# Kernel tuning notes

Measured on AMD Instinct MI355X. Metric: run time of the kernel, lower is better.

The kernel has to match this reference:

```python
import jax, jax.numpy as jnp
import numpy as np
from jax import lax

BS, H, W, C, V = 64, 32, 32, 684, 128
N, NP, Q, E, HID = 256, 512, 256, 256, 256  # n, n_prime, decoder_conv_filters, embedding_dim, hidden_size


def setup_inputs() -> dict:
    key = jax.random.key(0)
    ks = jax.random.split(key, 20)
    s = 0.02
    d = {}
    d["x"] = jax.random.randint(ks[0], (BS, 1), 0, V)
    d["hidden"] = jax.random.normal(ks[1], (1, BS, HID), jnp.float32)
    d["feature"] = jax.random.normal(ks[2], (BS, C, H, W), jnp.float32)
    d["alpha"] = jax.random.uniform(ks[3], (BS, 1, H * W), jnp.float32)
    d["emb"] = jax.random.normal(ks[4], (V, E), jnp.float32) * s
    d["gru1_wih"] = jax.random.normal(ks[5], (3 * HID, E), jnp.float32) * s
    d["gru1_whh"] = jax.random.normal(ks[6], (3 * HID, HID), jnp.float32) * s
    d["gru1_bih"] = jnp.zeros((3 * HID,), jnp.float32)
    d["gru1_bhh"] = jnp.zeros((3 * HID,), jnp.float32)
    d["gru2_wih"] = jax.random.normal(ks[7], (3 * HID, C), jnp.float32) * s
    d["gru2_whh"] = jax.random.normal(ks[8], (3 * HID, HID), jnp.float32) * s
    d["gru2_bih"] = jnp.zeros((3 * HID,), jnp.float32)
    d["gru2_bhh"] = jnp.zeros((3 * HID,), jnp.float32)
    d["convQ_w"] = jax.random.normal(ks[9], (Q, 1, 11, 11), jnp.float32) * s
    d["convQ_b"] = jnp.zeros((Q,), jnp.float32)
    d["Wa_w"] = jax.random.normal(ks[10], (NP, N), jnp.float32) * s
    d["Wa_b"] = jnp.zeros((NP,), jnp.float32)
    d["Ua_w"] = jax.random.normal(ks[11], (NP, C), jnp.float32) * s
    d["Ua_b"] = jnp.zeros((NP,), jnp.float32)
    d["Uf_w"] = jax.random.normal(ks[12], (NP, Q), jnp.float32) * s
    d["Uf_b"] = jnp.zeros((NP,), jnp.float32)
    d["Va_w"] = jax.random.normal(ks[13], (1, NP), jnp.float32) * s
    d["Va_b"] = jnp.zeros((1,), jnp.float32)
    d["Ws_w"] = jax.random.normal(ks[14], (E, HID), jnp.float32) * s
    d["Ws_b"] = jnp.zeros((E,), jnp.float32)
    d["Wc_w"] = jax.random.normal(ks[15], (E, C), jnp.float32) * s
    d["Wc_b"] = jnp.zeros((E,), jnp.float32)
    d["Wo_w"] = jax.random.normal(ks[16], (V, E // 2), jnp.float32) * s
    d["Wo_b"] = jnp.zeros((V,), jnp.float32)
    return d


def gru_step(x, h, w_ih, w_hh, b_ih, b_hh):
    """PyTorch nn.GRU single-step cell."""
    gi = x @ w_ih.T + b_ih
    gh = h @ w_hh.T + b_hh
    ir, iz, in_ = jnp.split(gi, 3, axis=-1)
    hr, hz, hn = jnp.split(gh, 3, axis=-1)
    r = jax.nn.sigmoid(ir + hr)
    z = jax.nn.sigmoid(iz + hz)
    n = jnp.tanh(in_ + r * hn)
    return (1.0 - z) * n + z * h


def reference(x, hidden, feature, alpha, emb,
              gru1_wih, gru1_whh, gru1_bih, gru1_bhh,
              gru2_wih, gru2_whh, gru2_bih, gru2_bhh,
              convQ_w, convQ_b, Wa_w, Wa_b, Ua_w, Ua_b,
              Uf_w, Uf_b, Va_w, Va_b, Ws_w, Ws_b, Wc_w, Wc_b, Wo_w, Wo_b):
    bs, c, h, w = feature.shape
    embedded = emb[x[:, 0]]                                   # [bs, E]
    pred = gru_step(embedded, hidden[0], gru1_wih, gru1_whh, gru1_bih, gru1_bhh)  # [bs, HID]

    # --- coverage attention ---
    beta = alpha.sum(1).reshape(bs, 1, h, w)                  # coverage map
    Fmap = lax.conv_general_dilated(beta, convQ_w, (1, 1), [(5, 5), (5, 5)],
                                    dimension_numbers=("NCHW", "OIHW", "NCHW"))
    Fmap = Fmap + convQ_b[None, :, None, None]                # [bs, Q, h, w]
    cover = jnp.einsum("bqhw,pq->bhwp", Fmap, Uf_w) + Uf_b    # [bs, h, w, NP]
    key_t = jnp.einsum("bchw,pc->bhwp", feature, Ua_w) + Ua_b # 1x1 conv_Ua
    query = pred @ Wa_w.T + Wa_b                              # [bs, NP]
    score = jnp.tanh(key_t + cover + query[:, None, None, :]) # [bs, h, w, NP]
    e_t = (jnp.einsum("bhwp,p->bhw", score, Va_w[0]) + Va_b[0]).reshape(bs, -1)
    e_exp = jnp.exp(e_t)                                      # faithful: exp/sum + 1e-8 (no max-shift)
    alpha_t = e_exp / (e_exp.sum(1, keepdims=True) + 1e-8)    # [bs, h*w]
    context = jnp.einsum("bcl,bl->bc", feature.reshape(bs, c, -1), alpha_t)  # [bs, C]

    # --- second GRU + output head ---
    h2 = gru_step(context, pred, gru2_wih, gru2_whh, gru2_bih, gru2_bhh)  # [bs, HID]
    o = embedded + (h2 @ Ws_w.T + Ws_b) + (context @ Wc_w.T + Wc_b)       # [bs, E]
    o = o.reshape(bs, -1, 2).max(-1)                                       # maxout pool 2
    logits = o @ Wo_w.T + Wo_b                                             # [bs, V]
    return logits, h2[:, None, :], alpha_t.reshape(bs, 1, h, w)
```

## Files before the change

kernel.cpp:

```cpp
#include <hip/hip_runtime.h>
#include <hip/hip_bf16.h>
#include <math.h>

#define BSZ 64
#define HGT 32
#define WID 32
#define HWN 1024
#define CCH 684
#define KP 704
#define VOC 128
#define NPP 512
#define QCH 256
#define EMB 256
#define HID 256
#define TAPP 128

typedef __attribute__((ext_vector_type(8))) short short8v;
typedef __attribute__((ext_vector_type(4))) float f32x4;

__device__ __forceinline__ float sigmoid_(float x) {
    return 1.0f / (1.0f + __expf(-x));
}
__device__ __forceinline__ float tanh_(float x) {
    x = fminf(fmaxf(x, -30.0f), 30.0f);
    float e = __expf(2.0f * x);
    return (e - 1.0f) / (e + 1.0f);
}
__device__ __forceinline__ unsigned short f2bf(float f) {
    unsigned int u = __float_as_uint(f);
    u = (u + 0x7FFFu + ((u >> 16) & 1u)) >> 16;
    return (unsigned short)u;
}

__global__ __launch_bounds__(256) void k_prep_ua(const float* __restrict__ Ua_w,
                                                 unsigned short* __restrict__ Ua_bf) {
    int p = blockIdx.x;
    for (int c = threadIdx.x; c < KP; c += 256) {
        unsigned short v = 0;
        if (c < CCH) v = f2bf(Ua_w[p * CCH + c]);
        Ua_bf[p * KP + c] = v;
    }
}

__global__ __launch_bounds__(256) void k_fold_w2(const float* __restrict__ Uf_w,
                                                 const float* __restrict__ Uf_b,
                                                 const float* __restrict__ convQ_w,
                                                 const float* __restrict__ convQ_b,
                                                 unsigned short* __restrict__ W2_bf,
                                                 float* __restrict__ covb) {
    int tap = blockIdx.x;
    int t = threadIdx.x;
    if (tap < TAPP) {
        for (int p = t; p < NPP; p += 256) {
            unsigned short v = 0;
            if (tap < 121) {
                float s = 0.f;
                for (int q = 0; q < QCH; q++) s += Uf_w[p * QCH + q] * convQ_w[q * 121 + tap];
                v = f2bf(s);
            }
            W2_bf[p * TAPP + tap] = v;
        }
    } else {
        for (int p = t; p < NPP; p += 256) {
            float s = Uf_b[p];
            for (int q = 0; q < QCH; q++) s += convQ_b[q] * Uf_w[p * QCH + q];
            covb[p] = s;
        }
    }
}

__global__ __launch_bounds__(256) void k_embed_gru1(const int* __restrict__ x,
                                                    const float* __restrict__ hidden,
                                                    const float* __restrict__ emb,
                                                    const float* __restrict__ w_ih,
                                                    const float* __restrict__ w_hh,
                                                    const float* __restrict__ b_ih,
                                                    const float* __restrict__ b_hh,
                                                    const float* __restrict__ Wa_w,
                                                    const float* __restrict__ Wa_b,
                                                    const float* __restrict__ covb,
                                                    const float* __restrict__ Ua_b,
                                                    float* __restrict__ ws_emb,
                                                    float* __restrict__ ws_pred,
                                                    float* __restrict__ ws_q0) {
    int b = blockIdx.x, t = threadIdx.x;
    __shared__ float se[EMB], sh[HID], sp[HID];
    int xi = x[b];
    se[t] = emb[xi * EMB + t];
    sh[t] = hidden[b * HID + t];
    __syncthreads();

    const float* wr = w_ih + (size_t)t * EMB;
    const float* wz = w_ih + (size_t)(t + 256) * EMB;
    const float* wn = w_ih + (size_t)(t + 512) * EMB;
    const float* vr = w_hh + (size_t)t * HID;
    const float* vz = w_hh + (size_t)(t + 256) * HID;
    const float* vn = w_hh + (size_t)(t + 512) * HID;
    float ir = 0, iz = 0, in_ = 0, hr = 0, hz = 0, hn = 0;
    for (int k = 0; k < EMB; k += 4) {
        float4 a0 = *(const float4*)(wr + k);
        float4 a1 = *(const float4*)(wz + k);
        float4 a2 = *(const float4*)(wn + k);
        float4 h0 = *(const float4*)(vr + k);
        float4 h1 = *(const float4*)(vz + k);
        float4 h2 = *(const float4*)(vn + k);
        float e0 = se[k], e1 = se[k + 1], e2 = se[k + 2], e3 = se[k + 3];
        float g0 = sh[k], g1 = sh[k + 1], g2 = sh[k + 2], g3 = sh[k + 3];
        ir += a0.x * e0 + a0.y * e1 + a0.z * e2 + a0.w * e3;
        iz += a1.x * e0 + a1.y * e1 + a1.z * e2 + a1.w * e3;
        in_ += a2.x * e0 + a2.y * e1 + a2.z * e2 + a2.w * e3;
        hr += h0.x * g0 + h0.y * g1 + h0.z * g2 + h0.w * g3;
        hz += h1.x * g0 + h1.y * g1 + h1.z * g2 + h1.w * g3;
        hn += h2.x * g0 + h2.y * g1 + h2.z * g2 + h2.w * g3;
    }
    float r = sigmoid_(ir + b_ih[t] + hr + b_hh[t]);
    float z = sigmoid_(iz + b_ih[256 + t] + hz + b_hh[256 + t]);
    float n = tanh_(in_ + b_ih[512 + t] + r * (hn + b_hh[512 + t]));
    float pred = (1.0f - z) * n + z * sh[t];
    ws_emb[b * EMB + t] = se[t];
    ws_pred[b * HID + t] = pred;
    sp[t] = pred;
    __syncthreads();

    for (int jj = 0; jj < 2; jj++) {
        int j = t + jj * 256;
        const float* wq = Wa_w + (size_t)j * HID;
        float q = Wa_b[j] + covb[j] + Ua_b[j];
        for (int k = 0; k < HID; k += 4) {
            float4 a = *(const float4*)(wq + k);
            q += a.x * sp[k] + a.y * sp[k + 1] + a.z * sp[k + 2] + a.w * sp[k + 3];
        }
        ws_q0[b * NPP + j] = q;
    }
}

__global__ __launch_bounds__(256, 2) void k_score(const float* __restrict__ feature,
                                                  const float* __restrict__ alpha,
                                                  const unsigned short* __restrict__ Ua_bf,
                                                  const unsigned short* __restrict__ W2_bf,
                                                  const float* __restrict__ ws_q0,
                                                  const float* __restrict__ Va_w,
                                                  const float* __restrict__ Va_b,
                                                  float* __restrict__ ws_et) {
    int rb = blockIdx.x;
    int b = blockIdx.y;
    int tid = threadIdx.x;
    int wv = tid >> 6;
    int lane = tid & 63;
    int li = lane & 15;
    int k08 = (lane >> 4) * 8;
    int pbase = wv * 128;

    __shared__ unsigned short s_a[64 * 40];
    __shared__ unsigned short s_a2[64 * 136];
    __shared__ float s_et[64];

    for (int idx = tid; idx < 64 * 128; idx += 256) {
        int hwl = idx >> 7, tap = idx & 127;
        unsigned short v = 0;
        if (tap < 121) {
            int ky = tap / 11, kx = tap - ky * 11;
            int hwg = rb * 64 + hwl;
            int y = (hwg >> 5) + ky - 5;
            int xx = (hwg & 31) + kx - 5;
            if (y >= 0 && y < HGT && xx >= 0 && xx < WID)
                v = f2bf(alpha[b * HWN + y * WID + xx]);
        }
        s_a2[hwl * 136 + tap] = v;
    }
    if (tid < 64) s_et[tid] = 0.f;

    f32x4 acc[4][8];
#pragma unroll
    for (int mt = 0; mt < 4; mt++)
#pragma unroll
        for (int nt = 0; nt < 8; nt++) acc[mt][nt] = (f32x4){0.f, 0.f, 0.f, 0.f};

    const float* fbase = feature + (size_t)b * CCH * HWN + rb * 64;
    int p2 = tid & 15, g = tid >> 4;
    unsigned int* s_a_u32 = (unsigned int*)s_a;

    for (int s = 0; s < 22; s++) {
        int c0 = s * 32;
        __syncthreads();
        {
            int c1 = c0 + 2 * p2;
            float4 f0 = make_float4(0.f, 0.f, 0.f, 0.f), f1 = f0;
            if (c1 < CCH) {
                f0 = *(const float4*)(fbase + (size_t)c1 * HWN + g * 4);
                f1 = *(const float4*)(fbase + (size_t)(c1 + 1) * HWN + g * 4);
            }
            s_a_u32[(g * 4 + 0) * 20 + p2] = (unsigned int)f2bf(f0.x) | ((unsigned int)f2bf(f1.x) << 16);
            s_a_u32[(g * 4 + 1) * 20 + p2] = (unsigned int)f2bf(f0.y) | ((unsigned int)f2bf(f1.y) << 16);
            s_a_u32[(g * 4 + 2) * 20 + p2] = (unsigned int)f2bf(f0.z) | ((unsigned int)f2bf(f1.z) << 16);
            s_a_u32[(g * 4 + 3) * 20 + p2] = (unsigned int)f2bf(f0.w) | ((unsigned int)f2bf(f1.w) << 16);
        }
        __syncthreads();
        short8v af[4];
#pragma unroll
        for (int mt = 0; mt < 4; mt++)
            af[mt] = *reinterpret_cast<const short8v*>(&s_a[(mt * 16 + li) * 40 + k08]);
#pragma unroll
        for (int nt = 0; nt < 8; nt++) {
            short8v bv = *reinterpret_cast<const short8v*>(
                Ua_bf + (size_t)(pbase + nt * 16 + li) * KP + c0 + k08);
#pragma unroll
            for (int mt = 0; mt < 4; mt++)
                acc[mt][nt] = __builtin_amdgcn_mfma_f32_16x16x32_bf16(af[mt], bv, acc[mt][nt], 0, 0, 0);
        }
    }

#pragma unroll
    for (int s = 0; s < 4; s++) {
        int t0 = s * 32;
        short8v af[4];
#pragma unroll
        for (int mt = 0; mt < 4; mt++)
            af[mt] = *reinterpret_cast<const short8v*>(&s_a2[(mt * 16 + li) * 136 + t0 + k08]);
#pragma unroll
        for (int nt = 0; nt < 8; nt++) {
            short8v bv = *reinterpret_cast<const short8v*>(
                W2_bf + (size_t)(pbase + nt * 16 + li) * TAPP + t0 + k08);
#pragma unroll
            for (int mt = 0; mt < 4; mt++)
                acc[mt][nt] = __builtin_amdgcn_mfma_f32_16x16x32_bf16(af[mt], bv, acc[mt][nt], 0, 0, 0);
        }
    }

    float part[4][4];
#pragma unroll
    for (int mt = 0; mt < 4; mt++)
#pragma unroll
        for (int r = 0; r < 4; r++) part[mt][r] = 0.f;

#pragma unroll
    for (int nt = 0; nt < 8; nt++) {
        int p = pbase + nt * 16 + li;
        float q0 = ws_q0[b * NPP + p];
        float va = Va_w[p];
#pragma unroll
        for (int mt = 0; mt < 4; mt++)
#pragma unroll
            for (int r = 0; r < 4; r++)
                part[mt][r] += va * tanh_(acc[mt][nt][r] + q0);
    }
#pragma unroll
    for (int mask = 1; mask <= 8; mask <<= 1)
#pragma unroll
        for (int mt = 0; mt < 4; mt++)
#pragma unroll
            for (int r = 0; r < 4; r++)
                part[mt][r] += __shfl_xor(part[mt][r], mask, 64);

    if (li == 0) {
        int rb4 = (lane >> 4) * 4;
#pragma unroll
        for (int mt = 0; mt < 4; mt++)
#pragma unroll
            for (int r = 0; r < 4; r++)
                atomicAdd(&s_et[mt * 16 + rb4 + r], part[mt][r]);
    }
    __syncthreads();
    if (tid < 64) ws_et[b * HWN + rb * 64 + tid] = s_et[tid] + Va_b[0];
}

__global__ __launch_bounds__(256) void k_softmax(const float* __restrict__ ws_et,
                                                 float* __restrict__ alpha_out) {
    int b = blockIdx.x, t = threadIdx.x;
    __shared__ float red[4];
    float e[4];
    float s = 0.f;
#pragma unroll
    for (int i = 0; i < 4; i++) {
        e[i] = expf(ws_et[b * HWN + t + i * 256]);
        s += e[i];
    }
#pragma unroll
    for (int off = 32; off >= 1; off >>= 1) s += __shfl_xor(s, off, 64);
    int wid = t >> 6;
    if ((t & 63) == 0) red[wid] = s;
    __syncthreads();
    float tot = red[0] + red[1] + red[2] + red[3] + 1e-8f;
    float inv = 1.0f / tot;
#pragma unroll
    for (int i = 0; i < 4; i++) alpha_out[b * HWN + t + i * 256] = e[i] * inv;
}

__global__ __launch_bounds__(256) void k_context(const float* __restrict__ feature,
                                                 const float* __restrict__ alpha_out,
                                                 float* __restrict__ ws_ctx) {
    int b = blockIdx.x;
    int c = blockIdx.y * 4 + (threadIdx.x >> 6);
    int lane = threadIdx.x & 63;
    const float* f = feature + ((size_t)b * CCH + c) * HWN;
    const float* a = alpha_out + b * HWN;
    float s = 0.f;
    for (int k = lane; k < HWN; k += 64) s += f[k] * a[k];
#pragma unroll
    for (int off = 32; off >= 1; off >>= 1) s += __shfl_xor(s, off, 64);
    if (lane == 0) ws_ctx[b * CCH + c] = s;
}

__global__ __launch_bounds__(256) void k_final(const float* __restrict__ ws_ctx,
                                               const float* __restrict__ ws_pred,
                                               const float* __restrict__ ws_emb,
                                               const float* __restrict__ w_ih2,
                                               const float* __restrict__ w_hh2,
                                               const float* __restrict__ b_ih2,
                                               const float* __restrict__ b_hh2,
                                               const float* __restrict__ Ws_w,
                                               const float* __restrict__ Ws_b,
                                               const float* __restrict__ Wc_w,
                                               const float* __restrict__ Wc_b,
                                               const float* __restrict__ Wo_w,
                                               const float* __restrict__ Wo_b,
                                               float* __restrict__ out_logits,
                                               float* __restrict__ out_h2) {
    int b = blockIdx.x, t = threadIdx.x;
    __shared__ float sc[CCH], sp[HID], semb[EMB], sh2[HID], so[EMB], som[VOC];
    for (int i = t; i < CCH; i += 256) sc[i] = ws_ctx[b * CCH + i];
    sp[t] = ws_pred[b * HID + t];
    semb[t] = ws_emb[b * EMB + t];
    __syncthreads();

    const float* wr = w_ih2 + (size_t)t * CCH;
    const float* wz = w_ih2 + (size_t)(t + 256) * CCH;
    const float* wn = w_ih2 + (size_t)(t + 512) * CCH;
    float ir = 0, iz = 0, in_ = 0;
    for (int k = 0; k < CCH; k += 4) {
        float4 a0 = *(const float4*)(wr + k);
        float4 a1 = *(const float4*)(wz + k);
        float4 a2 = *(const float4*)(wn + k);
        float c0 = sc[k], c1 = sc[k + 1], c2 = sc[k + 2], c3 = sc[k + 3];
        ir += a0.x * c0 + a0.y * c1 + a0.z * c2 + a0.w * c3;
        iz += a1.x * c0 + a1.y * c1 + a1.z * c2 + a1.w * c3;
        in_ += a2.x * c0 + a2.y * c1 + a2.z * c2 + a2.w * c3;
    }
    const float* vr = w_hh2 + (size_t)t * HID;
    const float* vz = w_hh2 + (size_t)(t + 256) * HID;
    const float* vn = w_hh2 + (size_t)(t + 512) * HID;
    float hr = 0, hz = 0, hn = 0;
    for (int k = 0; k < HID; k += 4) {
        float4 h0 = *(const float4*)(vr + k);
        float4 h1 = *(const float4*)(vz + k);
        float4 h2v = *(const float4*)(vn + k);
        float g0 = sp[k], g1 = sp[k + 1], g2 = sp[k + 2], g3 = sp[k + 3];
        hr += h0.x * g0 + h0.y * g1 + h0.z * g2 + h0.w * g3;
        hz += h1.x * g0 + h1.y * g1 + h1.z * g2 + h1.w * g3;
        hn += h2v.x * g0 + h2v.y * g1 + h2v.z * g2 + h2v.w * g3;
    }
    float rg = sigmoid_(ir + b_ih2[t] + hr + b_hh2[t]);
    float zg = sigmoid_(iz + b_ih2[256 + t] + hz + b_hh2[256 + t]);
    float ng = tanh_(in_ + b_ih2[512 + t] + rg * (hn + b_hh2[512 + t]));
    float h2 = (1.0f - zg) * ng + zg * sp[t];
    out_h2[b * HID + t] = h2;
    sh2[t] = h2;
    __syncthreads();

    const float* ws_row = Ws_w + (size_t)t * HID;
    const float* wc_row = Wc_w + (size_t)t * CCH;
    float o = semb[t] + Ws_b[t] + Wc_b[t];
    for (int k = 0; k < HID; k += 4) {
        float4 a = *(const float4*)(ws_row + k);
        o += a.x * sh2[k] + a.y * sh2[k + 1] + a.z * sh2[k + 2] + a.w * sh2[k + 3];
    }
    for (int k = 0; k < CCH; k += 4) {
        float4 a = *(const float4*)(wc_row + k);
        o += a.x * sc[k] + a.y * sc[k + 1] + a.z * sc[k + 2] + a.w * sc[k + 3];
    }
    so[t] = o;
    __syncthreads();
    if (t < VOC) som[t] = fmaxf(so[2 * t], so[2 * t + 1]);
    __syncthreads();
    if (t < VOC) {
        const float* wo_row = Wo_w + (size_t)t * VOC;
        float lg = Wo_b[t];
        for (int k = 0; k < VOC; k += 4) {
            float4 a = *(const float4*)(wo_row + k);
            lg += a.x * som[k] + a.y * som[k + 1] + a.z * som[k + 2] + a.w * som[k + 3];
        }
        out_logits[b * VOC + t] = lg;
    }
}

extern "C" void kernel_launch(void* const* d_in, const int* in_sizes, int n_in,
                              void* d_out, int out_size, void* d_ws, size_t ws_size,
                              hipStream_t stream) {
    const int* x = (const int*)d_in[0];
    const float* hidden = (const float*)d_in[1];
    const float* feature = (const float*)d_in[2];
    const float* alpha = (const float*)d_in[3];
    const float* emb = (const float*)d_in[4];
    const float* gru1_wih = (const float*)d_in[5];
    const float* gru1_whh = (const float*)d_in[6];
    const float* gru1_bih = (const float*)d_in[7];
    const float* gru1_bhh = (const float*)d_in[8];
    const float* gru2_wih = (const float*)d_in[9];
    const float* gru2_whh = (const float*)d_in[10];
    const float* gru2_bih = (const float*)d_in[11];
    const float* gru2_bhh = (const float*)d_in[12];
    const float* convQ_w = (const float*)d_in[13];
    const float* convQ_b = (const float*)d_in[14];
    const float* Wa_w = (const float*)d_in[15];
    const float* Wa_b = (const float*)d_in[16];
    const float* Ua_w = (const float*)d_in[17];
    const float* Ua_b = (const float*)d_in[18];
    const float* Uf_w = (const float*)d_in[19];
    const float* Uf_b = (const float*)d_in[20];
    const float* Va_w = (const float*)d_in[21];
    const float* Va_b = (const float*)d_in[22];
    const float* Ws_w = (const float*)d_in[23];
    const float* Ws_b = (const float*)d_in[24];
    const float* Wc_w = (const float*)d_in[25];
    const float* Wc_b = (const float*)d_in[26];
    const float* Wo_w = (const float*)d_in[27];
    const float* Wo_b = (const float*)d_in[28];

    float* out = (float*)d_out;
    float* out_logits = out;
    float* out_h2 = out + BSZ * VOC;
    float* out_alpha = out + BSZ * VOC + BSZ * HID;

    float* ws = (float*)d_ws;
    float* ws_emb = ws;
    float* ws_pred = ws + 16384;
    float* ws_q0 = ws + 32768;
    float* ws_et = ws + 65536;
    float* ws_ctx = ws + 131072;
    float* ws_covb = ws + 175104;
    unsigned short* Ua_bf = (unsigned short*)(ws + 175616);
    unsigned short* W2_bf = (unsigned short*)(ws + 355840);

    k_prep_ua<<<NPP, 256, 0, stream>>>(Ua_w, Ua_bf);
    k_fold_w2<<<TAPP + 1, 256, 0, stream>>>(Uf_w, Uf_b, convQ_w, convQ_b, W2_bf, ws_covb);
    k_embed_gru1<<<BSZ, 256, 0, stream>>>(x, hidden, emb, gru1_wih, gru1_whh,
                                          gru1_bih, gru1_bhh, Wa_w, Wa_b,
                                          ws_covb, Ua_b,
                                          ws_emb, ws_pred, ws_q0);
    k_score<<<dim3(16, BSZ), 256, 0, stream>>>(feature, alpha, Ua_bf, W2_bf,
                                               ws_q0, Va_w, Va_b, ws_et);
    k_softmax<<<BSZ, 256, 0, stream>>>(ws_et, out_alpha);
    k_context<<<dim3(BSZ, 171), 256, 0, stream>>>(feature, out_alpha, ws_ctx);
    k_final<<<BSZ, 256, 0, stream>>>(ws_ctx, ws_pred, ws_emb, gru2_wih, gru2_whh,
                                     gru2_bih, gru2_bhh, Ws_w, Ws_b, Wc_w, Wc_b,
                                     Wo_w, Wo_b, out_logits, out_h2);
}
```

Baseline: 693.2 us.

## Coalesce GRU matvecs with warp-per-row, stage full feature tile in LDS

The GRU, attention-query and output-head matvecs now give each weight row to one wavefront. Lanes read contiguous elements and the partial sums are reduced with shuffles, replacing the old one-row-per-thread strided loads that do not coalesce. k_fold_w2 now runs one block per output channel and keeps the Uf row in shared memory. The covb bias is reduced in parallel instead of in a serial loop. k_score moves to 512 threads: it converts the whole 64x684 feature tile to bf16 in LDS once instead of 22 staged chunks with barriers. Each wave now covers 64 instead of 128 projection columns, at the cost of about 108KB of LDS, which limits occupancy.

```diff
diff --git a/kernel.cpp b/kernel.cpp
--- a/kernel.cpp
+++ b/kernel.cpp
@@ -14,6 +14,7 @@
 #define EMB 256
 #define HID 256
 #define TAPP 128
+#define SAPAD 712
 
 typedef __attribute__((ext_vector_type(8))) short short8v;
 typedef __attribute__((ext_vector_type(4))) float f32x4;
@@ -48,25 +49,25 @@
                                                  const float* __restrict__ convQ_b,
                                                  unsigned short* __restrict__ W2_bf,
                                                  float* __restrict__ covb) {
-    int tap = blockIdx.x;
+    int p = blockIdx.x;
     int t = threadIdx.x;
-    if (tap < TAPP) {
-        for (int p = t; p < NPP; p += 256) {
-            unsigned short v = 0;
-            if (tap < 121) {
-                float s = 0.f;
-                for (int q = 0; q < QCH; q++) s += Uf_w[p * QCH + q] * convQ_w[q * 121 + tap];
-                v = f2bf(s);
-            }
-            W2_bf[p * TAPP + tap] = v;
-        }
-    } else {
-        for (int p = t; p < NPP; p += 256) {
-            float s = Uf_b[p];
-            for (int q = 0; q < QCH; q++) s += convQ_b[q] * Uf_w[p * QCH + q];
-            covb[p] = s;
-        }
-    }
+    __shared__ float s_uf[QCH];
+    __shared__ float s_red[4];
+    s_uf[t] = Uf_w[p * QCH + t];
+    __syncthreads();
+    if (t < TAPP) {
+        float s = 0.f;
+        if (t < 121) {
+            for (int q = 0; q < QCH; q++) s += s_uf[q] * convQ_w[q * 121 + t];
+        }
+        W2_bf[p * TAPP + t] = (t < 121) ? f2bf(s) : (unsigned short)0;
+    }
+    float v = convQ_b[t] * s_uf[t];
+#pragma unroll
+    for (int m = 32; m >= 1; m >>= 1) v += __shfl_xor(v, m, 64);
+    if ((t & 63) == 0) s_red[t >> 6] = v;
+    __syncthreads();
+    if (t == 0) covb[p] = Uf_b[p] + s_red[0] + s_red[1] + s_red[2] + s_red[3];
 }
 
 __global__ __launch_bounds__(256) void k_embed_gru1(const int* __restrict__ x,
@@ -84,57 +85,50 @@
                                                     float* __restrict__ ws_pred,
                                                     float* __restrict__ ws_q0) {
     int b = blockIdx.x, t = threadIdx.x;
-    __shared__ float se[EMB], sh[HID], sp[HID];
-    int xi = x[b];
-    se[t] = emb[xi * EMB + t];
+    int wv = t >> 6, lane = t & 63;
+    __shared__ float se[EMB], sh[HID], gi[768], gh[768], sp[HID];
+    se[t] = emb[x[b] * EMB + t];
     sh[t] = hidden[b * HID + t];
     __syncthreads();
 
-    const float* wr = w_ih + (size_t)t * EMB;
-    const float* wz = w_ih + (size_t)(t + 256) * EMB;
-    const float* wn = w_ih + (size_t)(t + 512) * EMB;
-    const float* vr = w_hh + (size_t)t * HID;
-    const float* vz = w_hh + (size_t)(t + 256) * HID;
-    const float* vn = w_hh + (size_t)(t + 512) * HID;
-    float ir = 0, iz = 0, in_ = 0, hr = 0, hz = 0, hn = 0;
-    for (int k = 0; k < EMB; k += 4) {
-        float4 a0 = *(const float4*)(wr + k);
-        float4 a1 = *(const float4*)(wz + k);
-        float4 a2 = *(const float4*)(wn + k);
-        float4 h0 = *(const float4*)(vr + k);
-        float4 h1 = *(const float4*)(vz + k);
-        float4 h2 = *(const float4*)(vn + k);
-        float e0 = se[k], e1 = se[k + 1], e2 = se[k + 2], e3 = se[k + 3];
-        float g0 = sh[k], g1 = sh[k + 1], g2 = sh[k + 2], g3 = sh[k + 3];
-        ir += a0.x * e0 + a0.y * e1 + a0.z * e2 + a0.w * e3;
-        iz += a1.x * e0 + a1.y * e1 + a1.z * e2 + a1.w * e3;
-        in_ += a2.x * e0 + a2.y * e1 + a2.z * e2 + a2.w * e3;
-        hr += h0.x * g0 + h0.y * g1 + h0.z * g2 + h0.w * g3;
-        hz += h1.x * g0 + h1.y * g1 + h1.z * g2 + h1.w * g3;
-        hn += h2.x * g0 + h2.y * g1 + h2.z * g2 + h2.w * g3;
-    }
-    float r = sigmoid_(ir + b_ih[t] + hr + b_hh[t]);
-    float z = sigmoid_(iz + b_ih[256 + t] + hz + b_hh[256 + t]);
-    float n = tanh_(in_ + b_ih[512 + t] + r * (hn + b_hh[512 + t]));
+    for (int i = 0; i < 192; i++) {
+        int j = wv * 192 + i;
+        const float* wi = w_ih + (size_t)j * EMB;
+        const float* wh = w_hh + (size_t)j * HID;
+        float s1 = wi[lane] * se[lane] + wi[lane + 64] * se[lane + 64] +
+                   wi[lane + 128] * se[lane + 128] + wi[lane + 192] * se[lane + 192];
+        float s2 = wh[lane] * sh[lane] + wh[lane + 64] * sh[lane + 64] +
+                   wh[lane + 128] * sh[lane + 128] + wh[lane + 192] * sh[lane + 192];
+#pragma unroll
+        for (int m = 32; m >= 1; m >>= 1) {
+            s1 += __shfl_xor(s1, m, 64);
+            s2 += __shfl_xor(s2, m, 64);
+        }
+        if (lane == 0) { gi[j] = s1; gh[j] = s2; }
+    }
+    __syncthreads();
+
+    float r = sigmoid_(gi[t] + b_ih[t] + gh[t] + b_hh[t]);
+    float z = sigmoid_(gi[256 + t] + b_ih[256 + t] + gh[256 + t] + b_hh[256 + t]);
+    float n = tanh_(gi[512 + t] + b_ih[512 + t] + r * (gh[512 + t] + b_hh[512 + t]));
     float pred = (1.0f - z) * n + z * sh[t];
     ws_emb[b * EMB + t] = se[t];
     ws_pred[b * HID + t] = pred;
     sp[t] = pred;
     __syncthreads();
 
-    for (int jj = 0; jj < 2; jj++) {
-        int j = t + jj * 256;
+    for (int i = 0; i < 128; i++) {
+        int j = wv * 128 + i;
         const float* wq = Wa_w + (size_t)j * HID;
-        float q = Wa_b[j] + covb[j] + Ua_b[j];
-        for (int k = 0; k < HID; k += 4) {
-            float4 a = *(const float4*)(wq + k);
-            q += a.x * sp[k] + a.y * sp[k + 1] + a.z * sp[k + 2] + a.w * sp[k + 3];
-        }
-        ws_q0[b * NPP + j] = q;
-    }
-}
-
-__global__ __launch_bounds__(256, 2) void k_score(const float* __restrict__ feature,
+        float q = wq[lane] * sp[lane] + wq[lane + 64] * sp[lane + 64] +
+                  wq[lane + 128] * sp[lane + 128] + wq[lane + 192] * sp[lane + 192];
+#pragma unroll
+        for (int m = 32; m >= 1; m >>= 1) q += __shfl_xor(q, m, 64);
+        if (lane == 0) ws_q0[b * NPP + j] = q + Wa_b[j] + covb[j] + Ua_b[j];
+    }
+}
+
+__global__ __launch_bounds__(512, 2) void k_score(const float* __restrict__ feature,
                                                   const float* __restrict__ alpha,
                                                   const unsigned short* __restrict__ Ua_bf,
                                                   const unsigned short* __restrict__ W2_bf,
@@ -149,13 +143,22 @@
     int lane = tid & 63;
     int li = lane & 15;
     int k08 = (lane >> 4) * 8;
-    int pbase = wv * 128;
-
-    __shared__ unsigned short s_a[64 * 40];
+    int pbase = wv * 64;
+
+    __shared__ unsigned short s_a[64 * SAPAD];
     __shared__ unsigned short s_a2[64 * 136];
     __shared__ float s_et[64];
 
-    for (int idx = tid; idx < 64 * 128; idx += 256) {
+    const float* fbase = feature + (size_t)b * CCH * HWN + rb * 64;
+    for (int idx = tid; idx < 64 * CCH; idx += 512) {
+        int c = idx >> 6, hw = idx & 63;
+        s_a[hw * SAPAD + c] = f2bf(fbase[(size_t)c * HWN + hw]);
+    }
+    for (int idx = tid; idx < 64 * (SAPAD - CCH); idx += 512) {
+        int hw = idx / (SAPAD - CCH), c = CCH + idx % (SAPAD - CCH);
+        s_a[hw * SAPAD + c] = 0;
+    }
+    for (int idx = tid; idx < 64 * 128; idx += 512) {
         int hwl = idx >> 7, tap = idx & 127;
         unsigned short v = 0;
         if (tap < 121) {
@@ -169,39 +172,22 @@
         s_a2[hwl * 136 + tap] = v;
     }
     if (tid < 64) s_et[tid] = 0.f;
-
-    f32x4 acc[4][8];
+    __syncthreads();
+
+    f32x4 acc[4][4];
 #pragma unroll
     for (int mt = 0; mt < 4; mt++)
 #pragma unroll
-        for (int nt = 0; nt < 8; nt++) acc[mt][nt] = (f32x4){0.f, 0.f, 0.f, 0.f};
-
-    const float* fbase = feature + (size_t)b * CCH * HWN + rb * 64;
-    int p2 = tid & 15, g = tid >> 4;
-    unsigned int* s_a_u32 = (unsigned int*)s_a;
+        for (int nt = 0; nt < 4; nt++) acc[mt][nt] = (f32x4){0.f, 0.f, 0.f, 0.f};
 
     for (int s = 0; s < 22; s++) {
         int c0 = s * 32;
-        __syncthreads();
-        {
-            int c1 = c0 + 2 * p2;
-            float4 f0 = make_float4(0.f, 0.f, 0.f, 0.f), f1 = f0;
-            if (c1 < CCH) {
-                f0 = *(const float4*)(fbase + (size_t)c1 * HWN + g * 4);
-                f1 = *(const float4*)(fbase + (size_t)(c1 + 1) * HWN + g * 4);
-            }
-            s_a_u32[(g * 4 + 0) * 20 + p2] = (unsigned int)f2bf(f0.x) | ((unsigned int)f2bf(f1.x) << 16);
-            s_a_u32[(g * 4 + 1) * 20 + p2] = (unsigned int)f2bf(f0.y) | ((unsigned int)f2bf(f1.y) << 16);
-            s_a_u32[(g * 4 + 2) * 20 + p2] = (unsigned int)f2bf(f0.z) | ((unsigned int)f2bf(f1.z) << 16);
-            s_a_u32[(g * 4 + 3) * 20 + p2] = (unsigned int)f2bf(f0.w) | ((unsigned int)f2bf(f1.w) << 16);
-        }
-        __syncthreads();
         short8v af[4];
 #pragma unroll
         for (int mt = 0; mt < 4; mt++)
-            af[mt] = *reinterpret_cast<const short8v*>(&s_a[(mt * 16 + li) * 40 + k08]);
-#pragma unroll
-        for (int nt = 0; nt < 8; nt++) {
+            af[mt] = *reinterpret_cast<const short8v*>(&s_a[(mt * 16 + li) * SAPAD + c0 + k08]);
+#pragma unroll
+        for (int nt = 0; nt < 4; nt++) {
             short8v bv = *reinterpret_cast<const short8v*>(
                 Ua_bf + (size_t)(pbase + nt * 16 + li) * KP + c0 + k08);
 #pragma unroll
@@ -218,7 +204,7 @@
         for (int mt = 0; mt < 4; mt++)
             af[mt] = *reinterpret_cast<const short8v*>(&s_a2[(mt * 16 + li) * 136 + t0 + k08]);
 #pragma unroll
-        for (int nt = 0; nt < 8; nt++) {
+        for (int nt = 0; nt < 4; nt++) {
             short8v bv = *reinterpret_cast<const short8v*>(
                 W2_bf + (size_t)(pbase + nt * 16 + li) * TAPP + t0 + k08);
 #pragma unroll
@@ -234,7 +220,7 @@
         for (int r = 0; r < 4; r++) part[mt][r] = 0.f;
 
 #pragma unroll
-    for (int nt = 0; nt < 8; nt++) {
+    for (int nt = 0; nt < 4; nt++) {
         int p = pbase + nt * 16 + li;
         float q0 = ws_q0[b * NPP + p];
         float va = Va_w[p];
@@ -317,69 +303,60 @@
                                                float* __restrict__ out_logits,
                                                float* __restrict__ out_h2) {
     int b = blockIdx.x, t = threadIdx.x;
-    __shared__ float sc[CCH], sp[HID], semb[EMB], sh2[HID], so[EMB], som[VOC];
+    int wv = t >> 6, lane = t & 63;
+    __shared__ float sc[CCH], sp[HID], semb[EMB], gi2[768], gh2[768], sh2[HID], so[EMB], som[VOC];
     for (int i = t; i < CCH; i += 256) sc[i] = ws_ctx[b * CCH + i];
     sp[t] = ws_pred[b * HID + t];
     semb[t] = ws_emb[b * EMB + t];
     __syncthreads();
 
-    const float* wr = w_ih2 + (size_t)t * CCH;
-    const float* wz = w_ih2 + (size_t)(t + 256) * CCH;
-    const float* wn = w_ih2 + (size_t)(t + 512) * CCH;
-    float ir = 0, iz = 0, in_ = 0;
-    for (int k = 0; k < CCH; k += 4) {
-        float4 a0 = *(const float4*)(wr + k);
-        float4 a1 = *(const float4*)(wz + k);
-        float4 a2 = *(const float4*)(wn + k);
-        float c0 = sc[k], c1 = sc[k + 1], c2 = sc[k + 2], c3 = sc[k + 3];
-        ir += a0.x * c0 + a0.y * c1 + a0.z * c2 + a0.w * c3;
-        iz += a1.x * c0 + a1.y * c1 + a1.z * c2 + a1.w * c3;
-        in_ += a2.x * c0 + a2.y * c1 + a2.z * c2 + a2.w * c3;
-    }
-    const float* vr = w_hh2 + (size_t)t * HID;
-    const float* vz = w_hh2 + (size_t)(t + 256) * HID;
-    const float* vn = w_hh2 + (size_t)(t + 512) * HID;
-    float hr = 0, hz = 0, hn = 0;
-    for (int k = 0; k < HID; k += 4) {
-        float4 h0 = *(const float4*)(vr + k);
-        float4 h1 = *(const float4*)(vz + k);
-        float4 h2v = *(const float4*)(vn + k);
-        float g0 = sp[k], g1 = sp[k + 1], g2 = sp[k + 2], g3 = sp[k + 3];
-        hr += h0.x * g0 + h0.y * g1 + h0.z * g2 + h0.w * g3;
-        hz += h1.x * g0 + h1.y * g1 + h1.z * g2 + h1.w * g3;
-        hn += h2v.x * g0 + h2v.y * g1 + h2v.z * g2 + h2v.w * g3;
-    }
-    float rg = sigmoid_(ir + b_ih2[t] + hr + b_hh2[t]);
-    float zg = sigmoid_(iz + b_ih2[256 + t] + hz + b_hh2[256 + t]);
-    float ng = tanh_(in_ + b_ih2[512 + t] + rg * (hn + b_hh2[512 + t]));
+    for (int i = 0; i < 192; i++) {
+        int j = wv * 192 + i;
+        const float* wi = w_ih2 + (size_t)j * CCH;
+        const float* wh = w_hh2 + (size_t)j * HID;
+        float s1 = 0.f;
+        for (int kk = lane; kk < CCH; kk += 64) s1 += wi[kk] * sc[kk];
+        float s2 = wh[lane] * sp[lane] + wh[lane + 64] * sp[lane + 64] +
+                   wh[lane + 128] * sp[lane + 128] + wh[lane + 192] * sp[lane + 192];
+#pragma unroll
+        for (int m = 32; m >= 1; m >>= 1) {
+            s1 += __shfl_xor(s1, m, 64);
+            s2 += __shfl_xor(s2, m, 64);
+        }
+        if (lane == 0) { gi2[j] = s1; gh2[j] = s2; }
+    }
+    __syncthreads();
+
+    float rg = sigmoid_(gi2[t] + b_ih2[t] + gh2[t] + b_hh2[t]);
+    float zg = sigmoid_(gi2[256 + t] + b_ih2[256 + t] + gh2[256 + t] + b_hh2[256 + t]);
+    float ng = tanh_(gi2[512 + t] + b_ih2[512 + t] + rg * (gh2[512 + t] + b_hh2[512 + t]));
     float h2 = (1.0f - zg) * ng + zg * sp[t];
     out_h2[b * HID + t] = h2;
     sh2[t] = h2;
     __syncthreads();
 
-    const float* ws_row = Ws_w + (size_t)t * HID;
-    const float* wc_row = Wc_w + (size_t)t * CCH;
-    float o = semb[t] + Ws_b[t] + Wc_b[t];
-    for (int k = 0; k < HID; k += 4) {
-        float4 a = *(const float4*)(ws_row + k);
-        o += a.x * sh2[k] + a.y * sh2[k + 1] + a.z * sh2[k + 2] + a.w * sh2[k + 3];
-    }
-    for (int k = 0; k < CCH; k += 4) {
-        float4 a = *(const float4*)(wc_row + k);
-        o += a.x * sc[k] + a.y * sc[k + 1] + a.z * sc[k + 2] + a.w * sc[k + 3];
-    }
-    so[t] = o;
+    for (int i = 0; i < 64; i++) {
+        int j = wv * 64 + i;
+        const float* wsr = Ws_w + (size_t)j * HID;
+        const float* wcr = Wc_w + (size_t)j * CCH;
+        float s = wsr[lane] * sh2[lane] + wsr[lane + 64] * sh2[lane + 64] +
+                  wsr[lane + 128] * sh2[lane + 128] + wsr[lane + 192] * sh2[lane + 192];
+        for (int kk = lane; kk < CCH; kk += 64) s += wcr[kk] * sc[kk];
+#pragma unroll
+        for (int m = 32; m >= 1; m >>= 1) s += __shfl_xor(s, m, 64);
+        if (lane == 0) so[j] = s + semb[j] + Ws_b[j] + Wc_b[j];
+    }
     __syncthreads();
     if (t < VOC) som[t] = fmaxf(so[2 * t], so[2 * t + 1]);
     __syncthreads();
-    if (t < VOC) {
-        const float* wo_row = Wo_w + (size_t)t * VOC;
-        float lg = Wo_b[t];
-        for (int k = 0; k < VOC; k += 4) {
-            float4 a = *(const float4*)(wo_row + k);
-            lg += a.x * som[k] + a.y * som[k + 1] + a.z * som[k + 2] + a.w * som[k + 3];
-        }
-        out_logits[b * VOC + t] = lg;
+
+    for (int i = 0; i < 32; i++) {
+        int j = wv * 32 + i;
+        const float* wo = Wo_w + (size_t)j * VOC;
+        float s = wo[lane] * som[lane] + wo[lane + 64] * som[lane + 64];
+#pragma unroll
+        for (int m = 32; m >= 1; m >>= 1) s += __shfl_xor(s, m, 64);
+        if (lane == 0) out_logits[b * VOC + j] = s + Wo_b[j];
     }
 }
 
@@ -432,12 +409,12 @@
     unsigned short* W2_bf = (unsigned short*)(ws + 355840);
 
     k_prep_ua<<<NPP, 256, 0, stream>>>(Ua_w, Ua_bf);
-    k_fold_w2<<<TAPP + 1, 256, 0, stream>>>(Uf_w, Uf_b, convQ_w, convQ_b, W2_bf, ws_covb);
+    k_fold_w2<<<NPP, 256, 0, stream>>>(Uf_w, Uf_b, convQ_w, convQ_b, W2_bf, ws_covb);
     k_embed_gru1<<<BSZ, 256, 0, stream>>>(x, hidden, emb, gru1_wih, gru1_whh,
                                           gru1_bih, gru1_bhh, Wa_w, Wa_b,
                                           ws_covb, Ua_b,
                                           ws_emb, ws_pred, ws_q0);
-    k_score<<<dim3(16, BSZ), 256, 0, stream>>>(feature, alpha, Ua_bf, W2_bf,
+    k_score<<<dim3(16, BSZ), 512, 0, stream>>>(feature, alpha, Ua_bf, W2_bf,
                                                ws_q0, Va_w, Va_b, ws_et);
     k_softmax<<<BSZ, 256, 0, stream>>>(ws_et, out_alpha);
     k_context<<<dim3(BSZ, 171), 256, 0, stream>>>(feature, out_alpha, ws_ctx);
```

New measurement: 1.855 ms. +167.6%, slower.
